# Performance work log

Measured on AMD Instinct MI355X. Metric: run time of the kernel, lower is better.

Reference implementation:

```python
import jax, jax.numpy as jnp
import numpy as np

N_NODES = 100000
N_EDGES = 3200000


def gcn_conv(x, W, b, src, dst, n_nodes):
    # x: [N, Fin] -> [N, Fout]; PyG GCNConv: linear, add self-loops,
    # symmetric norm D^-1/2 A_hat D^-1/2, sum-aggregate over incoming edges, + bias
    h = x @ W  # [N, Fout]
    loop = jnp.arange(n_nodes, dtype=src.dtype)
    src2 = jnp.concatenate([src, loop])
    dst2 = jnp.concatenate([dst, loop])
    deg = jax.ops.segment_sum(jnp.ones_like(dst2, dtype=h.dtype), dst2, num_segments=n_nodes)
    dinv = jnp.where(deg > 0, jax.lax.rsqrt(deg), 0.0)
    norm = dinv[src2] * dinv[dst2]  # [E+N]
    msgs = h[src2] * norm[:, None]  # gather + scale
    out = jax.ops.segment_sum(msgs, dst2, num_segments=n_nodes)  # scatter-add
    return out + b


def setup_inputs() -> dict:
    key = jax.random.key(0)
    k1, k2, k3, k4 = jax.random.split(key, 4)
    x = jax.random.normal(k1, (N_NODES, 16), dtype=jnp.float32)
    edge_index = jax.random.randint(k2, (2, N_EDGES), 0, N_NODES, dtype=jnp.int64)
    W1 = jax.random.normal(k3, (16, 32), dtype=jnp.float32) * (1.0 / np.sqrt(16))
    b1 = jnp.zeros((32,), dtype=jnp.float32)
    W2 = jax.random.normal(k4, (32, 3), dtype=jnp.float32) * (1.0 / np.sqrt(32))
    b2 = jnp.zeros((3,), dtype=jnp.float32)
    return {"x": x, "edge_index": edge_index, "W1": W1, "b1": b1, "W2": W2, "b2": b2}


def reference(x, edge_index, W1, b1, W2, b2):
    src, dst = edge_index[0], edge_index[1]
    n = x.shape[0]
    h = gcn_conv(x, W1, b1, src, dst, n)
    h = jax.nn.relu(h)
    h = gcn_conv(h, W2, b2, src, dst, n)
    return jax.nn.log_softmax(h, axis=1)
```

## Files before the change

### kernel.cpp

```cpp
#include <hip/hip_runtime.h>
#include <math.h>


#define NN 100000
#define NE 3200000
#define BSH 7
#define NPB 128
#define NB  ((NN + NPB - 1) / NPB)
#define EPB 12544
#define CAP 6144
#define SCAP 5632

__device__ __forceinline__ float bl(unsigned u) { return __uint_as_float(u << 16); }
__device__ __forceinline__ float bh(unsigned u) { return __uint_as_float(u & 0xFFFF0000u); }
__device__ __forceinline__ unsigned rne(float f) {
    unsigned u = __float_as_uint(f);
    return (u + 0x7FFFu + ((u >> 16) & 1u)) >> 16;
}

typedef int vint4 __attribute__((ext_vector_type(4)));
typedef float floatx2 __attribute__((ext_vector_type(2)));

#define FP8SCALE 8.0f
#define FP8INV   0.125f


__global__ void __launch_bounds__(256) k_zero(int* __restrict__ bcur) {
    int t = blockIdx.x * 256 + threadIdx.x;
    if (t < NB) bcur[t] = 0;
}

__global__ void __launch_bounds__(1024) k_partition(
        const int* __restrict__ src, const int* __restrict__ dst,
        int* __restrict__ bcur, unsigned int* __restrict__ ebuf, int E) {
    __shared__ int hist[NB];
    __shared__ int lbase[NB];
    __shared__ int gbase[NB];
    __shared__ int lcur[NB];
    __shared__ unsigned int sebuf[EPB];
    __shared__ unsigned short sbkt[EPB];
    __shared__ int wsum[16];
    int tid = threadIdx.x;
    int e0 = blockIdx.x * EPB;
    int e1 = min(e0 + EPB, E);
    int cnt = e1 - e0;
    int cnt4 = cnt >> 2;
    if (tid < NB) { hist[tid] = 0; lcur[tid] = 0; }
    __syncthreads();
    const vint4* d4 = (const vint4*)(dst + e0);
    vint4 dc[4];
#pragma unroll
    for (int r = 0; r < 4; r++) {
        int i4 = r * 1024 + tid;
        if (i4 < cnt4) {
            dc[r] = d4[i4];
            atomicAdd(&hist[dc[r].x >> BSH], 1);
            atomicAdd(&hist[dc[r].y >> BSH], 1);
            atomicAdd(&hist[dc[r].z >> BSH], 1);
            atomicAdd(&hist[dc[r].w >> BSH], 1);
        }
    }
    __syncthreads();
    int lane = tid & 63, w = tid >> 6;
    {
        int v = (tid < NB) ? hist[tid] : 0;
        int incl = v;
#pragma unroll
        for (int off = 1; off < 64; off <<= 1) {
            int u = __shfl_up(incl, off);
            if (lane >= off) incl += u;
        }
        if (lane == 63) wsum[w] = incl;
        __syncthreads();
        int woff = 0;
#pragma unroll
        for (int k = 0; k < 16; k++) woff += (k < w) ? wsum[k] : 0;
        int excl = incl - v + woff;
        if (tid < NB) {
            lbase[tid] = excl;
            gbase[tid] = tid * CAP + (v ? atomicAdd(&bcur[tid], v) : 0);
        }
        __syncthreads();
    }
    const vint4* s4 = (const vint4*)(src + e0);
#pragma unroll
    for (int r = 0; r < 4; r++) {
        int i4 = r * 1024 + tid;
        if (i4 < cnt4) {
            vint4 sv = s4[i4];
            int d, b, p;
            d = dc[r].x; b = d >> BSH; p = lbase[b] + atomicAdd(&lcur[b], 1);
            sebuf[p] = (unsigned)sv.x | ((unsigned)(d & (NPB - 1)) << 20);
            sbkt[p] = (unsigned short)b;
            d = dc[r].y; b = d >> BSH; p = lbase[b] + atomicAdd(&lcur[b], 1);
            sebuf[p] = (unsigned)sv.y | ((unsigned)(d & (NPB - 1)) << 20);
            sbkt[p] = (unsigned short)b;
            d = dc[r].z; b = d >> BSH; p = lbase[b] + atomicAdd(&lcur[b], 1);
            sebuf[p] = (unsigned)sv.z | ((unsigned)(d & (NPB - 1)) << 20);
            sbkt[p] = (unsigned short)b;
            d = dc[r].w; b = d >> BSH; p = lbase[b] + atomicAdd(&lcur[b], 1);
            sebuf[p] = (unsigned)sv.w | ((unsigned)(d & (NPB - 1)) << 20);
            sbkt[p] = (unsigned short)b;
        }
    }
    __syncthreads();
    for (int p = tid; p < cnt; p += 1024) {
        int b = sbkt[p];
        ebuf[gbase[b] + (p - lbase[b])] = sebuf[p];
    }
}

__global__ void __launch_bounds__(256) k_B(
        const unsigned int* __restrict__ ebuf, const int* __restrict__ bcur,
        const float* __restrict__ x, int* __restrict__ deg,
        unsigned int* __restrict__ xsb, int N) {
    __shared__ int hist[NPB];
    int b = blockIdx.x, tid = threadIdx.x;
    int beg = b * CAP, cnt = bcur[b];
    int cnt4 = cnt >> 2;
    if (tid < NPB) hist[tid] = 0;
    __syncthreads();
    const uint4* e4 = (const uint4*)(ebuf + beg);
    for (int j4 = tid; j4 < cnt4; j4 += 256) {
        uint4 pv = e4[j4];
        atomicAdd(&hist[pv.x >> 20], 1);
        atomicAdd(&hist[pv.y >> 20], 1);
        atomicAdd(&hist[pv.z >> 20], 1);
        atomicAdd(&hist[pv.w >> 20], 1);
    }
    for (int j = (cnt4 << 2) + tid; j < cnt; j += 256)
        atomicAdd(&hist[ebuf[beg + j] >> 20], 1);
    __syncthreads();
    if (tid < NPB) {
        int node = b * NPB + tid;
        if (node < N) {
            int v = hist[tid];
            deg[node] = v;
            float di = rsqrtf((float)(v + 1));
            float s = di * FP8SCALE;
            const float4* x4 = (const float4*)(x + (size_t)node * 16);
            float4 A = x4[0], Bv = x4[1], Cv = x4[2], Dv = x4[3];
            unsigned d0, d1, d2, d3;
            d0 = __builtin_amdgcn_cvt_pk_fp8_f32(A.x * s, A.y * s, 0, false);
            d0 = __builtin_amdgcn_cvt_pk_fp8_f32(A.z * s, A.w * s, d0, true);
            d1 = __builtin_amdgcn_cvt_pk_fp8_f32(Bv.x * s, Bv.y * s, 0, false);
            d1 = __builtin_amdgcn_cvt_pk_fp8_f32(Bv.z * s, Bv.w * s, d1, true);
            d2 = __builtin_amdgcn_cvt_pk_fp8_f32(Cv.x * s, Cv.y * s, 0, false);
            d2 = __builtin_amdgcn_cvt_pk_fp8_f32(Cv.z * s, Cv.w * s, d2, true);
            d3 = __builtin_amdgcn_cvt_pk_fp8_f32(Dv.x * s, Dv.y * s, 0, false);
            d3 = __builtin_amdgcn_cvt_pk_fp8_f32(Dv.z * s, Dv.w * s, d3, true);
            uint2 lo, hi;
            lo.x = d0; lo.y = d1;
            hi.x = d2; hi.y = d3;
            ((uint2*)xsb)[node] = lo;
            ((uint2*)(xsb + 2 * (size_t)NN))[node] = hi;
        }
    }
}

__global__ void __launch_bounds__(512) k_L1(
        const unsigned int* __restrict__ ebuf, const int* __restrict__ bcur,
        const int* __restrict__ deg, const unsigned int* __restrict__ xsb,
        const float* __restrict__ W1, const float* __restrict__ b1,
        const float* __restrict__ W2, unsigned int* __restrict__ g2b, int N) {
    __shared__ int scol[SCAP];
    __shared__ float sacc[NPB][17];
    __shared__ int sdeg[NPB];
    __shared__ int base[NPB];
    __shared__ int lcur[NPB];
    __shared__ float sdinv[NPB];
    __shared__ float W1s[512];
    __shared__ float W2s[96];
    __shared__ float b1s[32];
    __shared__ int wsum[2];
    int b = blockIdx.x, tid = threadIdx.x;
    int beg = b * CAP;
    int cnt = bcur[b];
    int cl = min(cnt, SCAP);
    int cl4 = cl >> 2;
    W1s[tid] = W1[tid];
    if (tid < 96) W2s[tid] = W2[tid];
    if (tid < 32) b1s[tid] = b1[tid];
    int lane = tid & 63, w = tid >> 6;
    int v = 0;
    if (tid < NPB) {
        int node = b * NPB + tid;
        v = (node < N) ? deg[node] : 0;
        sdeg[tid] = v;
        lcur[tid] = 0;
        sdinv[tid] = rsqrtf((float)(v + 1));
    }
    int incl = v;
#pragma unroll
    for (int off = 1; off < 64; off <<= 1) {
        int u = __shfl_up(incl, off);
        if (lane >= off) incl += u;
    }
    if (tid < NPB && lane == 63) wsum[w] = incl;
    __syncthreads();
    if (tid < NPB) base[tid] = incl - v + ((w == 1) ? wsum[0] : 0);
    __syncthreads();
    const uint4* e4 = (const uint4*)(ebuf + beg);
    for (int j4 = tid; j4 < cl4; j4 += 512) {
        uint4 pv = e4[j4];
        int dl, pos;
        dl = (int)(pv.x >> 20); pos = base[dl] + atomicAdd(&lcur[dl], 1);
        if (pos < SCAP) scol[pos] = (int)(pv.x & 0xFFFFF);
        dl = (int)(pv.y >> 20); pos = base[dl] + atomicAdd(&lcur[dl], 1);
        if (pos < SCAP) scol[pos] = (int)(pv.y & 0xFFFFF);
        dl = (int)(pv.z >> 20); pos = base[dl] + atomicAdd(&lcur[dl], 1);
        if (pos < SCAP) scol[pos] = (int)(pv.z & 0xFFFFF);
        dl = (int)(pv.w >> 20); pos = base[dl] + atomicAdd(&lcur[dl], 1);
        if (pos < SCAP) scol[pos] = (int)(pv.w & 0xFFFFF);
    }
    for (int j = (cl4 << 2) + tid; j < cl; j += 512) {
        unsigned pe = ebuf[beg + j];
        int dl = (int)(pe >> 20);
        int pos = base[dl] + atomicAdd(&lcur[dl], 1);
        if (pos < SCAP) scol[pos] = (int)(pe & 0xFFFFF);
    }
    __syncthreads();
    {
        int g = tid >> 4;
        int lq = tid & 15;
        int r = lq >> 1, c = lq & 1;
        const uint2* xlo = (const uint2*)xsb;
        const uint2* xhi = (const uint2*)(xsb + 2 * (size_t)NN);
        const uint2* xbc = c ? xhi : xlo;
#pragma unroll
        for (int p = 0; p < 4; p++) {
            int nib = p * 32 + g;
            int jb = base[nib];
            int je = jb + sdeg[nib];
            float a0 = 0.f, a1 = 0.f, a2 = 0.f, a3 = 0.f;
            float a4 = 0.f, a5 = 0.f, a6 = 0.f, a7 = 0.f;
            int j = jb + r;
            while (j + 8 < je) {
                int s0 = scol[j], s1 = scol[j + 8];
                uint2 q0 = xbc[s0];
                uint2 q1 = xbc[s1];
                floatx2 f;
                f = __builtin_amdgcn_cvt_pk_f32_fp8(q0.x, false); a0 += f.x; a1 += f.y;
                f = __builtin_amdgcn_cvt_pk_f32_fp8(q0.x, true);  a2 += f.x; a3 += f.y;
                f = __builtin_amdgcn_cvt_pk_f32_fp8(q0.y, false); a4 += f.x; a5 += f.y;
                f = __builtin_amdgcn_cvt_pk_f32_fp8(q0.y, true);  a6 += f.x; a7 += f.y;
                f = __builtin_amdgcn_cvt_pk_f32_fp8(q1.x, false); a0 += f.x; a1 += f.y;
                f = __builtin_amdgcn_cvt_pk_f32_fp8(q1.x, true);  a2 += f.x; a3 += f.y;
                f = __builtin_amdgcn_cvt_pk_f32_fp8(q1.y, false); a4 += f.x; a5 += f.y;
                f = __builtin_amdgcn_cvt_pk_f32_fp8(q1.y, true);  a6 += f.x; a7 += f.y;
                j += 16;
            }
            if (j < je) {
                int s = scol[j];
                uint2 qq = xbc[s];
                floatx2 f;
                f = __builtin_amdgcn_cvt_pk_f32_fp8(qq.x, false); a0 += f.x; a1 += f.y;
                f = __builtin_amdgcn_cvt_pk_f32_fp8(qq.x, true);  a2 += f.x; a3 += f.y;
                f = __builtin_amdgcn_cvt_pk_f32_fp8(qq.y, false); a4 += f.x; a5 += f.y;
                f = __builtin_amdgcn_cvt_pk_f32_fp8(qq.y, true);  a6 += f.x; a7 += f.y;
            }
#pragma unroll
            for (int off = 8; off >= 2; off >>= 1) {
                a0 += __shfl_down(a0, off);
                a1 += __shfl_down(a1, off);
                a2 += __shfl_down(a2, off);
                a3 += __shfl_down(a3, off);
                a4 += __shfl_down(a4, off);
                a5 += __shfl_down(a5, off);
                a6 += __shfl_down(a6, off);
                a7 += __shfl_down(a7, off);
            }
            if (lq < 2) {
                sacc[nib][c * 8 + 0] = a0; sacc[nib][c * 8 + 1] = a1;
                sacc[nib][c * 8 + 2] = a2; sacc[nib][c * 8 + 3] = a3;
                sacc[nib][c * 8 + 4] = a4; sacc[nib][c * 8 + 5] = a5;
                sacc[nib][c * 8 + 6] = a6; sacc[nib][c * 8 + 7] = a7;
            }
        }
    }
    __syncthreads();
    if (tid < NPB) {
        int node = b * NPB + tid;
        if (node < N) {
            float di = sdinv[tid];
            const uint2* xlo = (const uint2*)xsb;
            const uint2* xhi = (const uint2*)(xsb + 2 * (size_t)NN);
            uint2 sl = xlo[node], sh = xhi[node];
            floatx2 e0 = __builtin_amdgcn_cvt_pk_f32_fp8(sl.x, false);
            floatx2 e1 = __builtin_amdgcn_cvt_pk_f32_fp8(sl.x, true);
            floatx2 e2 = __builtin_amdgcn_cvt_pk_f32_fp8(sl.y, false);
            floatx2 e3 = __builtin_amdgcn_cvt_pk_f32_fp8(sl.y, true);
            floatx2 e4v = __builtin_amdgcn_cvt_pk_f32_fp8(sh.x, false);
            floatx2 e5 = __builtin_amdgcn_cvt_pk_f32_fp8(sh.x, true);
            floatx2 e6 = __builtin_amdgcn_cvt_pk_f32_fp8(sh.y, false);
            floatx2 e7 = __builtin_amdgcn_cvt_pk_f32_fp8(sh.y, true);
            float a[16] = {
                (sacc[tid][0] + e0.x) * FP8INV,  (sacc[tid][1] + e0.y) * FP8INV,
                (sacc[tid][2] + e1.x) * FP8INV,  (sacc[tid][3] + e1.y) * FP8INV,
                (sacc[tid][4] + e2.x) * FP8INV,  (sacc[tid][5] + e2.y) * FP8INV,
                (sacc[tid][6] + e3.x) * FP8INV,  (sacc[tid][7] + e3.y) * FP8INV,
                (sacc[tid][8] + e4v.x) * FP8INV, (sacc[tid][9] + e4v.y) * FP8INV,
                (sacc[tid][10] + e5.x) * FP8INV, (sacc[tid][11] + e5.y) * FP8INV,
                (sacc[tid][12] + e6.x) * FP8INV, (sacc[tid][13] + e6.y) * FP8INV,
                (sacc[tid][14] + e7.x) * FP8INV, (sacc[tid][15] + e7.y) * FP8INV};
            float p0 = 0.f, p1 = 0.f, p2 = 0.f;
#pragma unroll
            for (int jj = 0; jj < 32; jj++) {
                float o = 0.f;
#pragma unroll
                for (int k = 0; k < 16; k++) o = fmaf(a[k], W1s[k * 32 + jj], o);
                float z = fmaxf(fmaf(di, o, b1s[jj]), 0.f);
                p0 = fmaf(z, W2s[jj * 3 + 0], p0);
                p1 = fmaf(z, W2s[jj * 3 + 1], p1);
                p2 = fmaf(z, W2s[jj * 3 + 2], p2);
            }
            uint2 o;
            o.x = rne(p0 * di) | (rne(p1 * di) << 16);
            o.y = rne(p2 * di);
            ((uint2*)g2b)[node] = o;
        }
    }
}

__global__ void __launch_bounds__(512) k_L2(
        const unsigned int* __restrict__ ebuf, const int* __restrict__ bcur,
        const int* __restrict__ deg, const unsigned int* __restrict__ g2b,
        const float* __restrict__ b2, float* __restrict__ out, int N) {
    __shared__ int scol[SCAP];
    __shared__ int sdeg[NPB];
    __shared__ int base[NPB];
    __shared__ int lcur[NPB];
    __shared__ float sdinv[NPB];
    __shared__ int wsum[2];
    int b = blockIdx.x, tid = threadIdx.x;
    int beg = b * CAP;
    int cnt = bcur[b];
    int cl = min(cnt, SCAP);
    int cl4 = cl >> 2;
    int lane = tid & 63, w = tid >> 6;
    int v = 0;
    if (tid < NPB) {
        int node = b * NPB + tid;
        v = (node < N) ? deg[node] : 0;
        sdeg[tid] = v;
        lcur[tid] = 0;
        sdinv[tid] = rsqrtf((float)(v + 1));
    }
    int incl = v;
#pragma unroll
    for (int off = 1; off < 64; off <<= 1) {
        int u = __shfl_up(incl, off);
        if (lane >= off) incl += u;
    }
    if (tid < NPB && lane == 63) wsum[w] = incl;
    __syncthreads();
    if (tid < NPB) base[tid] = incl - v + ((w == 1) ? wsum[0] : 0);
    __syncthreads();
    const uint4* e4 = (const uint4*)(ebuf + beg);
    for (int j4 = tid; j4 < cl4; j4 += 512) {
        uint4 pv = e4[j4];
        int dl, pos;
        dl = (int)(pv.x >> 20); pos = base[dl] + atomicAdd(&lcur[dl], 1);
        if (pos < SCAP) scol[pos] = (int)(pv.x & 0xFFFFF);
        dl = (int)(pv.y >> 20); pos = base[dl] + atomicAdd(&lcur[dl], 1);
        if (pos < SCAP) scol[pos] = (int)(pv.y & 0xFFFFF);
        dl = (int)(pv.z >> 20); pos = base[dl] + atomicAdd(&lcur[dl], 1);
        if (pos < SCAP) scol[pos] = (int)(pv.z & 0xFFFFF);
        dl = (int)(pv.w >> 20); pos = base[dl] + atomicAdd(&lcur[dl], 1);
        if (pos < SCAP) scol[pos] = (int)(pv.w & 0xFFFFF);
    }
    for (int j = (cl4 << 2) + tid; j < cl; j += 512) {
        unsigned pe = ebuf[beg + j];
        int dl = (int)(pe >> 20);
        int pos = base[dl] + atomicAdd(&lcur[dl], 1);
        if (pos < SCAP) scol[pos] = (int)(pe & 0xFFFFF);
    }
    __syncthreads();
    {
        int lo = tid & 7;
        const uint2* gb = (const uint2*)g2b;
#pragma unroll
        for (int p = 0; p < 2; p++) {
            int nib = p * 64 + (tid >> 3);
            int node = b * NPB + nib;
            int jb = base[nib];
            int je = jb + sdeg[nib];
            float a0 = 0.f, a1 = 0.f, a2 = 0.f;
            int j = jb + lo;
            while (j + 8 < je) {
                uint2 v0 = gb[scol[j]];
                uint2 v1 = gb[scol[j + 8]];
                a0 += bl(v0.x); a1 += bh(v0.x); a2 += bl(v0.y);
                a0 += bl(v1.x); a1 += bh(v1.x); a2 += bl(v1.y);
                j += 16;
            }
            if (j < je) {
                uint2 vv = gb[scol[j]];
                a0 += bl(vv.x); a1 += bh(vv.x); a2 += bl(vv.y);
            }
#pragma unroll
            for (int off = 4; off >= 1; off >>= 1) {
                a0 += __shfl_down(a0, off);
                a1 += __shfl_down(a1, off);
                a2 += __shfl_down(a2, off);
            }
            if (lo == 0 && node < N) {
                float di = sdinv[nib];
                uint2 sv = gb[node];
                float v0 = fmaf(di, a0 + bl(sv.x), b2[0]);
                float v1 = fmaf(di, a1 + bh(sv.x), b2[1]);
                float v2 = fmaf(di, a2 + bl(sv.y), b2[2]);
                float m = fmaxf(v0, fmaxf(v1, v2));
                float lse = m + logf(expf(v0 - m) + expf(v1 - m) + expf(v2 - m));
                out[(size_t)node * 3 + 0] = v0 - lse;
                out[(size_t)node * 3 + 1] = v1 - lse;
                out[(size_t)node * 3 + 2] = v2 - lse;
            }
        }
    }
}


extern "C" void kernel_launch(void* const* d_in, const int* in_sizes, int n_in,
                              void* d_out, int out_size, void* d_ws, size_t ws_size,
                              hipStream_t stream) {
    const float* x  = (const float*)d_in[0];
    const int*   ei = (const int*)d_in[1];
    const float* W1 = (const float*)d_in[2];
    const float* b1 = (const float*)d_in[3];
    const float* W2 = (const float*)d_in[4];
    const float* b2 = (const float*)d_in[5];
    float* out = (float*)d_out;

    const int* src = ei;
    const int* dst = ei + NE;

    unsigned int* ebuf = (unsigned int*)d_ws;
    unsigned int* xsb  = ebuf + (size_t)NB * CAP;
    unsigned int* g2b  = xsb + (size_t)NN * 4;
    int*          deg  = (int*)(g2b + (size_t)NN * 2);
    int*          bcur = deg + NN;

    const int B = 256;
    int gbP = (NE + EPB - 1) / EPB;
    int gbZ = (NB + B - 1) / B;

    k_zero<<<gbZ, B, 0, stream>>>(bcur);
    k_partition<<<gbP, 1024, 0, stream>>>(src, dst, bcur, ebuf, NE);
    k_B<<<NB, B, 0, stream>>>(ebuf, bcur, x, deg, xsb, NN);
    k_L1<<<NB, 512, 0, stream>>>(ebuf, bcur, deg, xsb, W1, b1, W2, g2b, NN);
    k_L2<<<NB, 512, 0, stream>>>(ebuf, bcur, deg, g2b, b2, out, NN);
}
```

Baseline: 92.16 us.

## Split layer-1 aggregation into two passes over feature halves

Splits the layer-1 gather kernel into two kernels. The first aggregates the low 8 fp8 features and writes partial sums to a new global buffer. The second aggregates the high 8 features and finishes the dense transform. Each pass touches only half of the feature table, so the gathered working set (about 0.8 MB) is meant to stay in cache. The cost is rebuilding the per-block edge list twice, one extra launch, and a 3.2 MB partial-sum round trip.

```diff
diff --git a/kernel.cpp b/kernel.cpp
--- a/kernel.cpp
+++ b/kernel.cpp
@@ -158,13 +158,116 @@
     }
 }
 
-__global__ void __launch_bounds__(512) k_L1(
+__global__ void __launch_bounds__(512) k_L1a(
         const unsigned int* __restrict__ ebuf, const int* __restrict__ bcur,
         const int* __restrict__ deg, const unsigned int* __restrict__ xsb,
+        float* __restrict__ pacc, int N) {
+    __shared__ int scol[SCAP];
+    __shared__ int sdeg[NPB];
+    __shared__ int base[NPB];
+    __shared__ int lcur[NPB];
+    __shared__ int wsum[2];
+    int b = blockIdx.x, tid = threadIdx.x;
+    int beg = b * CAP;
+    int cnt = bcur[b];
+    int cl = min(cnt, SCAP);
+    int cl4 = cl >> 2;
+    int lane = tid & 63, w = tid >> 6;
+    int v = 0;
+    if (tid < NPB) {
+        int node = b * NPB + tid;
+        v = (node < N) ? deg[node] : 0;
+        sdeg[tid] = v;
+        lcur[tid] = 0;
+    }
+    int incl = v;
+#pragma unroll
+    for (int off = 1; off < 64; off <<= 1) {
+        int u = __shfl_up(incl, off);
+        if (lane >= off) incl += u;
+    }
+    if (tid < NPB && lane == 63) wsum[w] = incl;
+    __syncthreads();
+    if (tid < NPB) base[tid] = incl - v + ((w == 1) ? wsum[0] : 0);
+    __syncthreads();
+    const uint4* e4 = (const uint4*)(ebuf + beg);
+    for (int j4 = tid; j4 < cl4; j4 += 512) {
+        uint4 pv = e4[j4];
+        int dl, pos;
+        dl = (int)(pv.x >> 20); pos = base[dl] + atomicAdd(&lcur[dl], 1);
+        if (pos < SCAP) scol[pos] = (int)(pv.x & 0xFFFFF);
+        dl = (int)(pv.y >> 20); pos = base[dl] + atomicAdd(&lcur[dl], 1);
+        if (pos < SCAP) scol[pos] = (int)(pv.y & 0xFFFFF);
+        dl = (int)(pv.z >> 20); pos = base[dl] + atomicAdd(&lcur[dl], 1);
+        if (pos < SCAP) scol[pos] = (int)(pv.z & 0xFFFFF);
+        dl = (int)(pv.w >> 20); pos = base[dl] + atomicAdd(&lcur[dl], 1);
+        if (pos < SCAP) scol[pos] = (int)(pv.w & 0xFFFFF);
+    }
+    for (int j = (cl4 << 2) + tid; j < cl; j += 512) {
+        unsigned pe = ebuf[beg + j];
+        int dl = (int)(pe >> 20);
+        int pos = base[dl] + atomicAdd(&lcur[dl], 1);
+        if (pos < SCAP) scol[pos] = (int)(pe & 0xFFFFF);
+    }
+    __syncthreads();
+    {
+        int lo = tid & 7;
+        const uint2* xlo = (const uint2*)xsb;
+#pragma unroll
+        for (int p = 0; p < 2; p++) {
+            int nib = p * 64 + (tid >> 3);
+            int node = b * NPB + nib;
+            int jb = base[nib];
+            int je = jb + sdeg[nib];
+            float a0 = 0.f, a1 = 0.f, a2 = 0.f, a3 = 0.f;
+            float a4 = 0.f, a5 = 0.f, a6 = 0.f, a7 = 0.f;
+            int j = jb + lo;
+            while (j + 8 < je) {
+                uint2 q0 = xlo[scol[j]];
+                uint2 q1 = xlo[scol[j + 8]];
+                floatx2 f;
+                f = __builtin_amdgcn_cvt_pk_f32_fp8(q0.x, false); a0 += f.x; a1 += f.y;
+                f = __builtin_amdgcn_cvt_pk_f32_fp8(q0.x, true);  a2 += f.x; a3 += f.y;
+                f = __builtin_amdgcn_cvt_pk_f32_fp8(q0.y, false); a4 += f.x; a5 += f.y;
+                f = __builtin_amdgcn_cvt_pk_f32_fp8(q0.y, true);  a6 += f.x; a7 += f.y;
+                f = __builtin_amdgcn_cvt_pk_f32_fp8(q1.x, false); a0 += f.x; a1 += f.y;
+                f = __builtin_amdgcn_cvt_pk_f32_fp8(q1.x, true);  a2 += f.x; a3 += f.y;
+                f = __builtin_amdgcn_cvt_pk_f32_fp8(q1.y, false); a4 += f.x; a5 += f.y;
+                f = __builtin_amdgcn_cvt_pk_f32_fp8(q1.y, true);  a6 += f.x; a7 += f.y;
+                j += 16;
+            }
+            if (j < je) {
+                uint2 qq = xlo[scol[j]];
+                floatx2 f;
+                f = __builtin_amdgcn_cvt_pk_f32_fp8(qq.x, false); a0 += f.x; a1 += f.y;
+                f = __builtin_amdgcn_cvt_pk_f32_fp8(qq.x, true);  a2 += f.x; a3 += f.y;
+                f = __builtin_amdgcn_cvt_pk_f32_fp8(qq.y, false); a4 += f.x; a5 += f.y;
+                f = __builtin_amdgcn_cvt_pk_f32_fp8(qq.y, true);  a6 += f.x; a7 += f.y;
+            }
+#pragma unroll
+            for (int off = 4; off >= 1; off >>= 1) {
+                a0 += __shfl_down(a0, off); a1 += __shfl_down(a1, off);
+                a2 += __shfl_down(a2, off); a3 += __shfl_down(a3, off);
+                a4 += __shfl_down(a4, off); a5 += __shfl_down(a5, off);
+                a6 += __shfl_down(a6, off); a7 += __shfl_down(a7, off);
+            }
+            if (lo == 0 && node < N) {
+                float4* pp = (float4*)(pacc + (size_t)node * 8);
+                pp[0] = make_float4(a0, a1, a2, a3);
+                pp[1] = make_float4(a4, a5, a6, a7);
+            }
+        }
+    }
+}
+
+__global__ void __launch_bounds__(512) k_L1b(
+        const unsigned int* __restrict__ ebuf, const int* __restrict__ bcur,
+        const int* __restrict__ deg, const unsigned int* __restrict__ xsb,
+        const float* __restrict__ pacc,
         const float* __restrict__ W1, const float* __restrict__ b1,
         const float* __restrict__ W2, unsigned int* __restrict__ g2b, int N) {
     __shared__ int scol[SCAP];
-    __shared__ float sacc[NPB][17];
+    __shared__ float sacc[NPB][9];
     __shared__ int sdeg[NPB];
     __shared__ int base[NPB];
     __shared__ int lcur[NPB];
@@ -221,24 +324,19 @@
     }
     __syncthreads();
     {
-        int g = tid >> 4;
-        int lq = tid & 15;
-        int r = lq >> 1, c = lq & 1;
-        const uint2* xlo = (const uint2*)xsb;
+        int lo = tid & 7;
         const uint2* xhi = (const uint2*)(xsb + 2 * (size_t)NN);
-        const uint2* xbc = c ? xhi : xlo;
-#pragma unroll
-        for (int p = 0; p < 4; p++) {
-            int nib = p * 32 + g;
+#pragma unroll
+        for (int p = 0; p < 2; p++) {
+            int nib = p * 64 + (tid >> 3);
             int jb = base[nib];
             int je = jb + sdeg[nib];
             float a0 = 0.f, a1 = 0.f, a2 = 0.f, a3 = 0.f;
             float a4 = 0.f, a5 = 0.f, a6 = 0.f, a7 = 0.f;
-            int j = jb + r;
+            int j = jb + lo;
             while (j + 8 < je) {
-                int s0 = scol[j], s1 = scol[j + 8];
-                uint2 q0 = xbc[s0];
-                uint2 q1 = xbc[s1];
+                uint2 q0 = xhi[scol[j]];
+                uint2 q1 = xhi[scol[j + 8]];
                 floatx2 f;
                 f = __builtin_amdgcn_cvt_pk_f32_fp8(q0.x, false); a0 += f.x; a1 += f.y;
                 f = __builtin_amdgcn_cvt_pk_f32_fp8(q0.x, true);  a2 += f.x; a3 += f.y;
@@ -251,8 +349,7 @@
                 j += 16;
             }
             if (j < je) {
-                int s = scol[j];
-                uint2 qq = xbc[s];
+                uint2 qq = xhi[scol[j]];
                 floatx2 f;
                 f = __builtin_amdgcn_cvt_pk_f32_fp8(qq.x, false); a0 += f.x; a1 += f.y;
                 f = __builtin_amdgcn_cvt_pk_f32_fp8(qq.x, true);  a2 += f.x; a3 += f.y;
@@ -260,21 +357,17 @@
                 f = __builtin_amdgcn_cvt_pk_f32_fp8(qq.y, true);  a6 += f.x; a7 += f.y;
             }
 #pragma unroll
-            for (int off = 8; off >= 2; off >>= 1) {
-                a0 += __shfl_down(a0, off);
-                a1 += __shfl_down(a1, off);
-                a2 += __shfl_down(a2, off);
-                a3 += __shfl_down(a3, off);
-                a4 += __shfl_down(a4, off);
-                a5 += __shfl_down(a5, off);
-                a6 += __shfl_down(a6, off);
-                a7 += __shfl_down(a7, off);
-            }
-            if (lq < 2) {
-                sacc[nib][c * 8 + 0] = a0; sacc[nib][c * 8 + 1] = a1;
-                sacc[nib][c * 8 + 2] = a2; sacc[nib][c * 8 + 3] = a3;
-                sacc[nib][c * 8 + 4] = a4; sacc[nib][c * 8 + 5] = a5;
-                sacc[nib][c * 8 + 6] = a6; sacc[nib][c * 8 + 7] = a7;
+            for (int off = 4; off >= 1; off >>= 1) {
+                a0 += __shfl_down(a0, off); a1 += __shfl_down(a1, off);
+                a2 += __shfl_down(a2, off); a3 += __shfl_down(a3, off);
+                a4 += __shfl_down(a4, off); a5 += __shfl_down(a5, off);
+                a6 += __shfl_down(a6, off); a7 += __shfl_down(a7, off);
+            }
+            if (lo == 0) {
+                sacc[nib][0] = a0; sacc[nib][1] = a1;
+                sacc[nib][2] = a2; sacc[nib][3] = a3;
+                sacc[nib][4] = a4; sacc[nib][5] = a5;
+                sacc[nib][6] = a6; sacc[nib][7] = a7;
             }
         }
     }
@@ -286,6 +379,8 @@
             const uint2* xlo = (const uint2*)xsb;
             const uint2* xhi = (const uint2*)(xsb + 2 * (size_t)NN);
             uint2 sl = xlo[node], sh = xhi[node];
+            const float4* pp = (const float4*)(pacc + (size_t)node * 8);
+            float4 pl0 = pp[0], pl1 = pp[1];
             floatx2 e0 = __builtin_amdgcn_cvt_pk_f32_fp8(sl.x, false);
             floatx2 e1 = __builtin_amdgcn_cvt_pk_f32_fp8(sl.x, true);
             floatx2 e2 = __builtin_amdgcn_cvt_pk_f32_fp8(sl.y, false);
@@ -295,14 +390,14 @@
             floatx2 e6 = __builtin_amdgcn_cvt_pk_f32_fp8(sh.y, false);
             floatx2 e7 = __builtin_amdgcn_cvt_pk_f32_fp8(sh.y, true);
             float a[16] = {
-                (sacc[tid][0] + e0.x) * FP8INV,  (sacc[tid][1] + e0.y) * FP8INV,
-                (sacc[tid][2] + e1.x) * FP8INV,  (sacc[tid][3] + e1.y) * FP8INV,
-                (sacc[tid][4] + e2.x) * FP8INV,  (sacc[tid][5] + e2.y) * FP8INV,
-                (sacc[tid][6] + e3.x) * FP8INV,  (sacc[tid][7] + e3.y) * FP8INV,
-                (sacc[tid][8] + e4v.x) * FP8INV, (sacc[tid][9] + e4v.y) * FP8INV,
-                (sacc[tid][10] + e5.x) * FP8INV, (sacc[tid][11] + e5.y) * FP8INV,
-                (sacc[tid][12] + e6.x) * FP8INV, (sacc[tid][13] + e6.y) * FP8INV,
-                (sacc[tid][14] + e7.x) * FP8INV, (sacc[tid][15] + e7.y) * FP8INV};
+                (pl0.x + e0.x) * FP8INV,  (pl0.y + e0.y) * FP8INV,
+                (pl0.z + e1.x) * FP8INV,  (pl0.w + e1.y) * FP8INV,
+                (pl1.x + e2.x) * FP8INV,  (pl1.y + e2.y) * FP8INV,
+                (pl1.z + e3.x) * FP8INV,  (pl1.w + e3.y) * FP8INV,
+                (sacc[tid][0] + e4v.x) * FP8INV, (sacc[tid][1] + e4v.y) * FP8INV,
+                (sacc[tid][2] + e5.x) * FP8INV,  (sacc[tid][3] + e5.y) * FP8INV,
+                (sacc[tid][4] + e6.x) * FP8INV,  (sacc[tid][5] + e6.y) * FP8INV,
+                (sacc[tid][6] + e7.x) * FP8INV,  (sacc[tid][7] + e7.y) * FP8INV};
             float p0 = 0.f, p1 = 0.f, p2 = 0.f;
 #pragma unroll
             for (int jj = 0; jj < 32; jj++) {
@@ -438,7 +533,8 @@
     unsigned int* ebuf = (unsigned int*)d_ws;
     unsigned int* xsb  = ebuf + (size_t)NB * CAP;
     unsigned int* g2b  = xsb + (size_t)NN * 4;
-    int*          deg  = (int*)(g2b + (size_t)NN * 2);
+    float*        pacc = (float*)(g2b + (size_t)NN * 2);
+    int*          deg  = (int*)(pacc + (size_t)NN * 8);
     int*          bcur = deg + NN;
 
     const int B = 256;
@@ -448,6 +544,7 @@
     k_zero<<<gbZ, B, 0, stream>>>(bcur);
     k_partition<<<gbP, 1024, 0, stream>>>(src, dst, bcur, ebuf, NE);
     k_B<<<NB, B, 0, stream>>>(ebuf, bcur, x, deg, xsb, NN);
-    k_L1<<<NB, 512, 0, stream>>>(ebuf, bcur, deg, xsb, W1, b1, W2, g2b, NN);
+    k_L1a<<<NB, 512, 0, stream>>>(ebuf, bcur, deg, xsb, pacc, NN);
+    k_L1b<<<NB, 512, 0, stream>>>(ebuf, bcur, deg, xsb, pacc, W1, b1, W2, g2b, NN);
     k_L2<<<NB, 512, 0, stream>>>(ebuf, bcur, deg, g2b, b2, out, NN);
 }
```

New measurement: 97.28 us. 5.6% more time.
